# Optimization experiments

Hardware: AMD Instinct MI355X
Metric: run time of the kernel (lower is better)

Reference implementation:

```python
import jax, jax.numpy as jnp
import numpy as np

N_HEAD = 4

def setup_inputs() -> dict:
    key = jax.random.key(0)
    ks = jax.random.split(key, 10)
    B, N, C = 4, 16384, 256
    s = 1.0 / np.sqrt(C)
    inp = {
        'x': jax.random.normal(ks[0], (B, N, C), dtype=jnp.float32),
        'mask_x': jnp.ones((B, N), dtype=jnp.float32),
        'mask_y': jnp.ones((B, N), dtype=jnp.float32),
        'Wq': jax.random.normal(ks[1], (C, C), dtype=jnp.float32) * s,
        'bq': jnp.zeros((C,), dtype=jnp.float32),
        'Wk': jax.random.normal(ks[2], (C, C), dtype=jnp.float32) * s,
        'bk': jnp.zeros((C,), dtype=jnp.float32),
        'Wv': jax.random.normal(ks[3], (C, C), dtype=jnp.float32) * s,
        'bv': jnp.zeros((C,), dtype=jnp.float32),
        'Wp': jax.random.normal(ks[4], (C, C), dtype=jnp.float32) * s,
        'bp': jnp.zeros((C,), dtype=jnp.float32),
    }
    return inp

def reference(x, mask_x, mask_y, Wq, bq, Wk, bk, Wv, bv, Wp, bp):
    B, N, C = x.shape
    H = N_HEAD
    D = C // H
    # projections (y = x, self-attention path); weights stored [in, out]
    def split_heads(t):  # [B,N,C] -> [B,H,N,D]
        return t.reshape(B, N, H, D).transpose(0, 2, 1, 3)
    Q = split_heads(x @ Wq + bq)
    K = split_heads(x @ Wk + bk)
    V = split_heads(x @ Wv + bv)
    mx = mask_x[:, None, :, None]  # [B,1,N,1]
    my = mask_y[:, None, :, None]  # [B,1,M,1]
    K = K * my
    V = V * my
    # torch F.gelu default is exact (erf) gelu
    Q = jax.nn.gelu(Q, approximate=False) + 1.0
    K = jax.nn.gelu(K, approximate=False) + 1.0
    KV = jnp.einsum('bhmd,bhme->bhde', K, V)          # [B,H,D,D]
    K_sum = K.sum(axis=2, keepdims=True)               # [B,H,1,D]
    denom = jnp.sum(Q * K_sum, axis=-1, keepdims=True) # [B,H,N,1]
    attn_out = jnp.einsum('bhnd,bhde->bhne', Q, KV) / denom
    attn_out = attn_out * mx
    out = attn_out.transpose(0, 2, 1, 3).reshape(B, N, C)
    return out @ Wp + bp
```

## Files before the change

### kernel.cpp

```cpp
#include <hip/hip_runtime.h>
#include <hip/hip_bf16.h>
#include <cstdint>
#include <cstddef>

#define SEQ   16384
#define CHN   256

typedef __attribute__((ext_vector_type(8))) short  short8;
typedef __attribute__((ext_vector_type(4))) float  f32x4;

static __device__ __forceinline__ unsigned short f2bf(float f) {
    unsigned int u = __builtin_bit_cast(unsigned int, f);
    u += 0x7fffu + ((u >> 16) & 1u);
    return (unsigned short)(u >> 16);
}
static __device__ __forceinline__ float bf2f(unsigned short h) {
    unsigned int u = ((unsigned int)h) << 16;
    return __builtin_bit_cast(float, u);
}
static __device__ __forceinline__ float gelu_exact(float x) {
    return 0.5f * x * (1.0f + erff(x * 0.70710678118654752f));
}
static __device__ __forceinline__ int swz_us(int row, int kbyte) {
    return (row * 128 + (kbyte ^ ((row & 7) << 4))) >> 1;
}
static __device__ __forceinline__ int swzA(int row, int kbyte) {
    return (row * 512 + (kbyte ^ ((row & 7) << 4))) >> 1;
}

__global__ __launch_bounds__(256) void prep_kernel(
    const float* __restrict__ Wq, const float* __restrict__ Wk,
    const float* __restrict__ Wv, const float* __restrict__ Wp,
    unsigned short* __restrict__ Wqt, unsigned short* __restrict__ Wkt,
    unsigned short* __restrict__ Wvt, unsigned short* __restrict__ Wpt,
    float* __restrict__ KV, float* __restrict__ Ksum)
{
    const int idx = blockIdx.x * 256 + threadIdx.x;
    const int n = idx >> 8, k = idx & 255;
    const int src = k * 256 + n;
    Wqt[idx] = f2bf(Wq[src]);
    Wkt[idx] = f2bf(Wk[src]);
    Wvt[idx] = f2bf(Wv[src]);
    Wpt[idx] = f2bf(Wp[src]);
    KV[idx] = 0.0f;
    if (idx < 1024) Ksum[idx] = 0.0f;
}

__global__ __launch_bounds__(256) void qkv_gemm(
    const float* __restrict__ x, const float* __restrict__ my,
    const unsigned short* __restrict__ Wqt, const unsigned short* __restrict__ Wkt,
    const unsigned short* __restrict__ Wvt,
    const float* __restrict__ bq, const float* __restrict__ bk,
    const float* __restrict__ bv,
    unsigned short* __restrict__ Qb, unsigned short* __restrict__ Kb,
    unsigned short* __restrict__ Vb)
{
    __shared__ unsigned short As[128 * 256];
    __shared__ float mys[128];
    const int t = threadIdx.x;
    const long row0 = (long)blockIdx.x * 128;
    const int lane = t & 63, wave = t >> 6, wm = wave >> 1, wn = wave & 1;

    #pragma unroll
    for (int it = 0; it < 32; ++it) {
        const int idx = it * 256 + t;
        const int r = idx >> 6, c4 = (idx & 63) * 4;
        const float4 v = *(const float4*)(x + (row0 + r) * 256 + c4);
        uint2 pk;
        pk.x = (unsigned int)f2bf(v.x) | ((unsigned int)f2bf(v.y) << 16);
        pk.y = (unsigned int)f2bf(v.z) | ((unsigned int)f2bf(v.w) << 16);
        *(uint2*)&As[swzA(r, c4 * 2)] = pk;
    }
    if (t < 128) mys[t] = my[row0 + t];
    __syncthreads();

    #pragma unroll 1
    for (int ot = 0; ot < 6; ++ot) {
        const int mat  = ot >> 1;
        const int col0 = (ot & 1) * 128;
        const unsigned short* Wt = (mat == 0) ? Wqt : (mat == 1) ? Wkt : Wvt;
        const float* bias        = (mat == 0) ? bq  : (mat == 1) ? bk  : bv;
        unsigned short* Ob       = (mat == 0) ? Qb  : (mat == 1) ? Kb  : Vb;

        f32x4 acc[4][4];
        #pragma unroll
        for (int i = 0; i < 4; ++i)
            #pragma unroll
            for (int j = 0; j < 4; ++j) acc[i][j] = (f32x4)0.0f;

        #pragma unroll
        for (int kk = 0; kk < 8; ++kk) {
            const int ke = kk * 32 + (lane >> 4) * 8;
            short8 af[4], bfr[4];
            #pragma unroll
            for (int mi = 0; mi < 4; ++mi) {
                const int r = wm * 64 + mi * 16 + (lane & 15);
                af[mi] = *(const short8*)&As[swzA(r, ke * 2)];
            }
            #pragma unroll
            for (int ni = 0; ni < 4; ++ni) {
                const int n = col0 + wn * 64 + ni * 16 + (lane & 15);
                bfr[ni] = *(const short8*)(Wt + (size_t)n * 256 + ke);
            }
            #pragma unroll
            for (int mi = 0; mi < 4; ++mi)
                #pragma unroll
                for (int ni = 0; ni < 4; ++ni)
                    acc[mi][ni] = __builtin_amdgcn_mfma_f32_16x16x32_bf16(
                        af[mi], bfr[ni], acc[mi][ni], 0, 0, 0);
        }

        #pragma unroll
        for (int ni = 0; ni < 4; ++ni) {
            const int coll = col0 + wn * 64 + ni * 16 + (lane & 15);
            const float bc = bias[coll];
            #pragma unroll
            for (int mi = 0; mi < 4; ++mi) {
                const int lr0 = wm * 64 + mi * 16 + ((lane >> 4) << 2);
                #pragma unroll
                for (int r = 0; r < 4; ++r) {
                    const int lr = lr0 + r;
                    float val = acc[mi][ni][r] + bc;
                    if (mat == 0)      val = gelu_exact(val) + 1.0f;
                    else if (mat == 1) val = gelu_exact(val * mys[lr]) + 1.0f;
                    else               val = val * mys[lr];
                    Ob[(row0 + lr) * 256 + coll] = f2bf(val);
                }
            }
        }
    }
}

__global__ __launch_bounds__(256) void kv_reduce(
    const unsigned short* __restrict__ Kb, const unsigned short* __restrict__ Vb,
    float* __restrict__ KV, float* __restrict__ Ksum)
{
    __shared__ float kf[16][64];
    __shared__ float vf[16][64];
    const int t = threadIdx.x;
    const int bh = blockIdx.y;
    const long base = (long)(bh >> 2) * SEQ * 256 + (bh & 3) * 64;
    const long m0 = (long)blockIdx.x * 256;
    const int d0 = (t >> 4) * 4, e0 = (t & 15) * 4;
    const int sr = t >> 4, swhich = (t >> 3) & 1, sseg = t & 7;
    float acc[4][4] = {};
    float ks[4] = {};
    for (int it = 0; it < 16; ++it) {
        const long row = m0 + it * 16 + sr;
        const unsigned short* src = (swhich ? Vb : Kb) + base + row * 256 + sseg * 8;
        const uint4 raw = *(const uint4*)src;
        const unsigned short* rh = (const unsigned short*)&raw;
        float* dst = swhich ? &vf[sr][sseg * 8] : &kf[sr][sseg * 8];
        #pragma unroll
        for (int j = 0; j < 8; ++j) dst[j] = bf2f(rh[j]);
        __syncthreads();
        #pragma unroll
        for (int mm = 0; mm < 16; ++mm) {
            const float4 kd = *(const float4*)&kf[mm][d0];
            const float4 ve = *(const float4*)&vf[mm][e0];
            const float k4[4] = {kd.x, kd.y, kd.z, kd.w};
            const float v4[4] = {ve.x, ve.y, ve.z, ve.w};
            #pragma unroll
            for (int i = 0; i < 4; ++i)
                #pragma unroll
                for (int j = 0; j < 4; ++j) acc[i][j] += k4[i] * v4[j];
            if ((t & 15) == 0) {
                #pragma unroll
                for (int i = 0; i < 4; ++i) ks[i] += k4[i];
            }
        }
        __syncthreads();
    }
    #pragma unroll
    for (int i = 0; i < 4; ++i)
        #pragma unroll
        for (int j = 0; j < 4; ++j)
            atomicAdd(&KV[((size_t)bh * 64 + d0 + i) * 64 + e0 + j], acc[i][j]);
    if ((t & 15) == 0) {
        #pragma unroll
        for (int i = 0; i < 4; ++i) atomicAdd(&Ksum[bh * 64 + d0 + i], ks[i]);
    }
}

__global__ __launch_bounds__(256) void attn_kernel(
    const unsigned short* __restrict__ Qb, const float* __restrict__ KV,
    const float* __restrict__ Ksum, const float* __restrict__ mx,
    unsigned short* __restrict__ Ab)
{
    __shared__ unsigned short Qs[128 * 64];
    __shared__ unsigned short KVT[64 * 64];
    __shared__ float ksh[64];
    __shared__ float sden[128];
    const int t = threadIdx.x;
    const long row0 = (long)blockIdx.x * 128;
    const int b = (int)(row0 >> 14);
    const int lane = t & 63, wave = t >> 6, wm = wave >> 1, wn = wave & 1;

    for (int h = 0; h < 4; ++h) {
        const int bh = b * 4 + h;
        #pragma unroll
        for (int it = 0; it < 4; ++it) {
            const int idx = it * 256 + t;
            const int r = idx >> 3, c8 = (idx & 7) * 8;
            const uint4 v = *(const uint4*)(Qb + (row0 + r) * 256 + h * 64 + c8);
            *(uint4*)&Qs[swz_us(r, c8 * 2)] = v;
        }
        {
            const int e = t & 63, dg = t >> 6;
            #pragma unroll
            for (int i = 0; i < 16; ++i) {
                const int d = dg * 16 + i;
                const float v = KV[((size_t)bh * 64 + d) * 64 + e];
                KVT[(e * 128 + ((d * 2) ^ ((e & 7) << 4))) >> 1] = f2bf(v);
            }
        }
        if (t < 64) ksh[t] = Ksum[bh * 64 + t];
        __syncthreads();
        if (t < 128) {
            float s = 0.0f;
            for (int d = 0; d < 64; ++d)
                s += bf2f(Qs[swz_us(t, d * 2)]) * ksh[d];
            sden[t] = mx[row0 + t] / s;
        }
        __syncthreads();
        f32x4 acc[4][2];
        #pragma unroll
        for (int i = 0; i < 4; ++i) { acc[i][0] = (f32x4)0.0f; acc[i][1] = (f32x4)0.0f; }
        #pragma unroll
        for (int kk = 0; kk < 2; ++kk) {
            const int kbyte = kk * 64 + (lane >> 4) * 16;
            short8 af[4], bfr[2];
            #pragma unroll
            for (int mi = 0; mi < 4; ++mi) {
                const int r = wm * 64 + mi * 16 + (lane & 15);
                af[mi] = *(const short8*)&Qs[swz_us(r, kbyte)];
            }
            #pragma unroll
            for (int ni = 0; ni < 2; ++ni) {
                const int e = wn * 32 + ni * 16 + (lane & 15);
                bfr[ni] = *(const short8*)&KVT[swz_us(e, kbyte)];
            }
            #pragma unroll
            for (int mi = 0; mi < 4; ++mi)
                #pragma unroll
                for (int ni = 0; ni < 2; ++ni)
                    acc[mi][ni] = __builtin_amdgcn_mfma_f32_16x16x32_bf16(
                        af[mi], bfr[ni], acc[mi][ni], 0, 0, 0);
        }
        #pragma unroll
        for (int ni = 0; ni < 2; ++ni) {
            const int e = wn * 32 + ni * 16 + (lane & 15);
            #pragma unroll
            for (int mi = 0; mi < 4; ++mi) {
                const int lr0 = wm * 64 + mi * 16 + ((lane >> 4) << 2);
                #pragma unroll
                for (int r = 0; r < 4; ++r) {
                    const int lr = lr0 + r;
                    const float val = acc[mi][ni][r] * sden[lr];
                    Ab[(row0 + lr) * 256 + h * 64 + e] = f2bf(val);
                }
            }
        }
        __syncthreads();
    }
}

__global__ __launch_bounds__(256) void proj_gemm(
    const unsigned short* __restrict__ Ab, const unsigned short* __restrict__ Wpt,
    const float* __restrict__ bp, float* __restrict__ out)
{
    __shared__ unsigned short As[128 * 256];
    const int t = threadIdx.x;
    const long row0 = (long)blockIdx.x * 128;
    const int lane = t & 63, wave = t >> 6, wm = wave >> 1, wn = wave & 1;

    #pragma unroll
    for (int it = 0; it < 16; ++it) {
        const int idx = it * 256 + t;
        const int r = idx >> 5, c8 = (idx & 31) * 8;
        const uint4 v = *(const uint4*)(Ab + (row0 + r) * 256 + c8);
        *(uint4*)&As[swzA(r, c8 * 2)] = v;
    }
    __syncthreads();

    #pragma unroll 1
    for (int ct = 0; ct < 2; ++ct) {
        const int col0 = ct * 128;
        f32x4 acc[4][4];
        #pragma unroll
        for (int i = 0; i < 4; ++i)
            #pragma unroll
            for (int j = 0; j < 4; ++j) acc[i][j] = (f32x4)0.0f;

        #pragma unroll
        for (int kk = 0; kk < 8; ++kk) {
            const int ke = kk * 32 + (lane >> 4) * 8;
            short8 af[4], bfr[4];
            #pragma unroll
            for (int mi = 0; mi < 4; ++mi) {
                const int r = wm * 64 + mi * 16 + (lane & 15);
                af[mi] = *(const short8*)&As[swzA(r, ke * 2)];
            }
            #pragma unroll
            for (int ni = 0; ni < 4; ++ni) {
                const int n = col0 + wn * 64 + ni * 16 + (lane & 15);
                bfr[ni] = *(const short8*)(Wpt + (size_t)n * 256 + ke);
            }
            #pragma unroll
            for (int mi = 0; mi < 4; ++mi)
                #pragma unroll
                for (int ni = 0; ni < 4; ++ni)
                    acc[mi][ni] = __builtin_amdgcn_mfma_f32_16x16x32_bf16(
                        af[mi], bfr[ni], acc[mi][ni], 0, 0, 0);
        }

        #pragma unroll
        for (int ni = 0; ni < 4; ++ni) {
            const int coll = col0 + wn * 64 + ni * 16 + (lane & 15);
            const float bc = bp[coll];
            #pragma unroll
            for (int mi = 0; mi < 4; ++mi) {
                const int lr0 = wm * 64 + mi * 16 + ((lane >> 4) << 2);
                #pragma unroll
                for (int r = 0; r < 4; ++r) {
                    const long grow = row0 + lr0 + r;
                    out[grow * 256 + coll] = acc[mi][ni][r] + bc;
                }
            }
        }
    }
}

extern "C" void kernel_launch(void* const* d_in, const int* in_sizes, int n_in,
                              void* d_out, int out_size, void* d_ws, size_t ws_size,
                              hipStream_t stream)
{
    (void)in_sizes; (void)n_in; (void)out_size; (void)ws_size;
    const float* x  = (const float*)d_in[0];
    const float* mx = (const float*)d_in[1];
    const float* my = (const float*)d_in[2];
    const float* Wq = (const float*)d_in[3];
    const float* bq = (const float*)d_in[4];
    const float* Wk = (const float*)d_in[5];
    const float* bk = (const float*)d_in[6];
    const float* Wv = (const float*)d_in[7];
    const float* bv = (const float*)d_in[8];
    const float* Wp = (const float*)d_in[9];
    const float* bp = (const float*)d_in[10];
    float* out = (float*)d_out;

    const size_t nelem = (size_t)4 * SEQ * CHN;
    char* w = (char*)d_ws;
    unsigned short* Qb  = (unsigned short*)w; w += nelem * 2;
    unsigned short* Kb  = (unsigned short*)w; w += nelem * 2;
    unsigned short* Vb  = (unsigned short*)w; w += nelem * 2;
    unsigned short* Wqt = (unsigned short*)w; w += 131072;
    unsigned short* Wkt = (unsigned short*)w; w += 131072;
    unsigned short* Wvt = (unsigned short*)w; w += 131072;
    unsigned short* Wpt = (unsigned short*)w; w += 131072;
    float* KV   = (float*)w; w += 262144;
    float* Ksum = (float*)w; w += 4096;
    unsigned short* Ab = Kb;

    prep_kernel<<<256, 256, 0, stream>>>(Wq, Wk, Wv, Wp, Wqt, Wkt, Wvt, Wpt, KV, Ksum);
    qkv_gemm<<<512, 256, 0, stream>>>(x, my, Wqt, Wkt, Wvt, bq, bk, bv, Qb, Kb, Vb);
    kv_reduce<<<dim3(64, 16), 256, 0, stream>>>(Kb, Vb, KV, Ksum);
    attn_kernel<<<512, 256, 0, stream>>>(Qb, KV, Ksum, mx, Ab);
    proj_gemm<<<512, 256, 0, stream>>>(Ab, Wpt, bp, out);
}
```

Measured before the change: 416.4 us.

## Retile QKV and projection GEMMs with K-looped LDS tiles via global_load_lds

Adds a separate kernel that converts x to bf16 up front. The QKV and projection GEMMs are retiled so each workgroup computes one 128x128 output tile. Operand blocks of A and B (128x64 each) are staged into LDS per K step using global_load_lds, replacing the full-row A tile in LDS and direct global loads of the weights. Workgroups are interleaved across the 8 XCD slots and the grids grow to 3072 and 1024 blocks, to raise occupancy through smaller LDS use and to improve cache locality. The trade-offs are an extra write and read of x in bf16, repeated A-tile loads for each column tile, and LDS tiles with no swizzle that may cause bank conflicts.

After: 349.9 us. 1.19x faster.

```diff
diff --git a/kernel.cpp b/kernel.cpp
--- a/kernel.cpp
+++ b/kernel.cpp
@@ -9,6 +9,12 @@
 typedef __attribute__((ext_vector_type(8))) short  short8;
 typedef __attribute__((ext_vector_type(4))) float  f32x4;
 
+#define AS1 __attribute__((address_space(1)))
+#define AS3 __attribute__((address_space(3)))
+static __device__ __forceinline__ void gl_lds16(const void* g, void* l) {
+    __builtin_amdgcn_global_load_lds((const AS1 void*)g, (AS3 void*)l, 16, 0, 0);
+}
+
 static __device__ __forceinline__ unsigned short f2bf(float f) {
     unsigned int u = __builtin_bit_cast(unsigned int, f);
     u += 0x7fffu + ((u >> 16) & 1u);
@@ -24,83 +30,94 @@
 static __device__ __forceinline__ int swz_us(int row, int kbyte) {
     return (row * 128 + (kbyte ^ ((row & 7) << 4))) >> 1;
 }
-static __device__ __forceinline__ int swzA(int row, int kbyte) {
-    return (row * 512 + (kbyte ^ ((row & 7) << 4))) >> 1;
+
+__global__ __launch_bounds__(256) void cvt_kernel(
+    const float* __restrict__ x, unsigned short* __restrict__ xb)
+{
+    const int t0 = blockIdx.x * 256 + threadIdx.x;
+    #pragma unroll
+    for (int i = 0; i < 4; ++i) {
+        const long g = (long)t0 + (long)i * 524288;
+        const float4 a = *(const float4*)(x + g * 8);
+        const float4 b = *(const float4*)(x + g * 8 + 4);
+        uint4 pk;
+        pk.x = (unsigned int)f2bf(a.x) | ((unsigned int)f2bf(a.y) << 16);
+        pk.y = (unsigned int)f2bf(a.z) | ((unsigned int)f2bf(a.w) << 16);
+        pk.z = (unsigned int)f2bf(b.x) | ((unsigned int)f2bf(b.y) << 16);
+        pk.w = (unsigned int)f2bf(b.z) | ((unsigned int)f2bf(b.w) << 16);
+        *(uint4*)(xb + g * 8) = pk;
+    }
 }
 
 __global__ __launch_bounds__(256) void prep_kernel(
     const float* __restrict__ Wq, const float* __restrict__ Wk,
     const float* __restrict__ Wv, const float* __restrict__ Wp,
-    unsigned short* __restrict__ Wqt, unsigned short* __restrict__ Wkt,
-    unsigned short* __restrict__ Wvt, unsigned short* __restrict__ Wpt,
+    unsigned short* __restrict__ Wcat, unsigned short* __restrict__ Wpt,
     float* __restrict__ KV, float* __restrict__ Ksum)
 {
     const int idx = blockIdx.x * 256 + threadIdx.x;
     const int n = idx >> 8, k = idx & 255;
     const int src = k * 256 + n;
-    Wqt[idx] = f2bf(Wq[src]);
-    Wkt[idx] = f2bf(Wk[src]);
-    Wvt[idx] = f2bf(Wv[src]);
-    Wpt[idx] = f2bf(Wp[src]);
+    Wcat[idx]          = f2bf(Wq[src]);
+    Wcat[65536 + idx]  = f2bf(Wk[src]);
+    Wcat[131072 + idx] = f2bf(Wv[src]);
+    Wpt[idx]           = f2bf(Wp[src]);
     KV[idx] = 0.0f;
     if (idx < 1024) Ksum[idx] = 0.0f;
 }
 
 __global__ __launch_bounds__(256) void qkv_gemm(
-    const float* __restrict__ x, const float* __restrict__ my,
-    const unsigned short* __restrict__ Wqt, const unsigned short* __restrict__ Wkt,
-    const unsigned short* __restrict__ Wvt,
+    const unsigned short* __restrict__ xb, const float* __restrict__ my,
+    const unsigned short* __restrict__ Wcat,
     const float* __restrict__ bq, const float* __restrict__ bk,
     const float* __restrict__ bv,
     unsigned short* __restrict__ Qb, unsigned short* __restrict__ Kb,
     unsigned short* __restrict__ Vb)
 {
-    __shared__ unsigned short As[128 * 256];
+    __shared__ unsigned short As[128 * 64];
+    __shared__ unsigned short Bs[128 * 64];
     __shared__ float mys[128];
     const int t = threadIdx.x;
-    const long row0 = (long)blockIdx.x * 128;
+    const int nwg = 3072, phys = blockIdx.x;
+    const int l = (phys & 7) * (nwg >> 3) + (phys >> 3);
+    const int rt = l / 6, ct = l % 6;
+    const long row0 = (long)rt * 128;
+    const int  ncol0 = ct * 128;
+    const int  mat = ct >> 1;
     const int lane = t & 63, wave = t >> 6, wm = wave >> 1, wn = wave & 1;
 
-    #pragma unroll
-    for (int it = 0; it < 32; ++it) {
-        const int idx = it * 256 + t;
-        const int r = idx >> 6, c4 = (idx & 63) * 4;
-        const float4 v = *(const float4*)(x + (row0 + r) * 256 + c4);
-        uint2 pk;
-        pk.x = (unsigned int)f2bf(v.x) | ((unsigned int)f2bf(v.y) << 16);
-        pk.y = (unsigned int)f2bf(v.z) | ((unsigned int)f2bf(v.w) << 16);
-        *(uint2*)&As[swzA(r, c4 * 2)] = pk;
-    }
     if (t < 128) mys[t] = my[row0 + t];
-    __syncthreads();
-
-    #pragma unroll 1
-    for (int ot = 0; ot < 6; ++ot) {
-        const int mat  = ot >> 1;
-        const int col0 = (ot & 1) * 128;
-        const unsigned short* Wt = (mat == 0) ? Wqt : (mat == 1) ? Wkt : Wvt;
-        const float* bias        = (mat == 0) ? bq  : (mat == 1) ? bk  : bv;
-        unsigned short* Ob       = (mat == 0) ? Qb  : (mat == 1) ? Kb  : Vb;
-
-        f32x4 acc[4][4];
-        #pragma unroll
-        for (int i = 0; i < 4; ++i)
-            #pragma unroll
-            for (int j = 0; j < 4; ++j) acc[i][j] = (f32x4)0.0f;
-
-        #pragma unroll
-        for (int kk = 0; kk < 8; ++kk) {
-            const int ke = kk * 32 + (lane >> 4) * 8;
+
+    f32x4 acc[4][4];
+    #pragma unroll
+    for (int i = 0; i < 4; ++i)
+        #pragma unroll
+        for (int j = 0; j < 4; ++j) acc[i][j] = (f32x4)0.0f;
+
+    for (int k0 = 0; k0 < 256; k0 += 64) {
+        #pragma unroll
+        for (int i = 0; i < 4; ++i) {
+            const int c = i * 256 + t;
+            gl_lds16(xb + (row0 + (c >> 3)) * 256 + k0 + (c & 7) * 8, &As[c * 8]);
+        }
+        #pragma unroll
+        for (int i = 0; i < 4; ++i) {
+            const int c = i * 256 + t;
+            gl_lds16(Wcat + (size_t)(ncol0 + (c >> 3)) * 256 + k0 + (c & 7) * 8, &Bs[c * 8]);
+        }
+        __syncthreads();
+        #pragma unroll
+        for (int kk = 0; kk < 2; ++kk) {
             short8 af[4], bfr[4];
             #pragma unroll
             for (int mi = 0; mi < 4; ++mi) {
                 const int r = wm * 64 + mi * 16 + (lane & 15);
-                af[mi] = *(const short8*)&As[swzA(r, ke * 2)];
+                af[mi] = *(const short8*)&As[r * 64 + kk * 32 + (lane >> 4) * 8];
             }
             #pragma unroll
             for (int ni = 0; ni < 4; ++ni) {
-                const int n = col0 + wn * 64 + ni * 16 + (lane & 15);
-                bfr[ni] = *(const short8*)(Wt + (size_t)n * 256 + ke);
+                const int n = wn * 64 + ni * 16 + (lane & 15);
+                bfr[ni] = *(const short8*)&Bs[n * 64 + kk * 32 + (lane >> 4) * 8];
             }
             #pragma unroll
             for (int mi = 0; mi < 4; ++mi)
@@ -109,23 +126,27 @@
                     acc[mi][ni] = __builtin_amdgcn_mfma_f32_16x16x32_bf16(
                         af[mi], bfr[ni], acc[mi][ni], 0, 0, 0);
         }
-
-        #pragma unroll
-        for (int ni = 0; ni < 4; ++ni) {
-            const int coll = col0 + wn * 64 + ni * 16 + (lane & 15);
-            const float bc = bias[coll];
-            #pragma unroll
-            for (int mi = 0; mi < 4; ++mi) {
-                const int lr0 = wm * 64 + mi * 16 + ((lane >> 4) << 2);
-                #pragma unroll
-                for (int r = 0; r < 4; ++r) {
-                    const int lr = lr0 + r;
-                    float val = acc[mi][ni][r] + bc;
-                    if (mat == 0)      val = gelu_exact(val) + 1.0f;
-                    else if (mat == 1) val = gelu_exact(val * mys[lr]) + 1.0f;
-                    else               val = val * mys[lr];
-                    Ob[(row0 + lr) * 256 + coll] = f2bf(val);
-                }
+        __syncthreads();
+    }
+
+    const float* bias  = (mat == 0) ? bq : (mat == 1) ? bk : bv;
+    unsigned short* Ob = (mat == 0) ? Qb : (mat == 1) ? Kb : Vb;
+    const int col0 = (ct & 1) * 128;
+    #pragma unroll
+    for (int ni = 0; ni < 4; ++ni) {
+        const int coll = col0 + wn * 64 + ni * 16 + (lane & 15);
+        const float bc = bias[coll];
+        #pragma unroll
+        for (int mi = 0; mi < 4; ++mi) {
+            const int lr0 = wm * 64 + mi * 16 + ((lane >> 4) << 2);
+            #pragma unroll
+            for (int r = 0; r < 4; ++r) {
+                const int lr = lr0 + r;
+                float val = acc[mi][ni][r] + bc;
+                if (mat == 0)      val = gelu_exact(val) + 1.0f;
+                else if (mat == 1) val = gelu_exact(val * mys[lr]) + 1.0f;
+                else               val = val * mys[lr];
+                Ob[(row0 + lr) * 256 + coll] = f2bf(val);
             }
         }
     }
@@ -269,42 +290,46 @@
     const unsigned short* __restrict__ Ab, const unsigned short* __restrict__ Wpt,
     const float* __restrict__ bp, float* __restrict__ out)
 {
-    __shared__ unsigned short As[128 * 256];
+    __shared__ unsigned short As[128 * 64];
+    __shared__ unsigned short Bs[128 * 64];
     const int t = threadIdx.x;
-    const long row0 = (long)blockIdx.x * 128;
+    const int nwg = 1024, phys = blockIdx.x;
+    const int l = (phys & 7) * (nwg >> 3) + (phys >> 3);
+    const int rt = l >> 1, ct = l & 1;
+    const long row0 = (long)rt * 128;
+    const int col0 = ct * 128;
     const int lane = t & 63, wave = t >> 6, wm = wave >> 1, wn = wave & 1;
 
-    #pragma unroll
-    for (int it = 0; it < 16; ++it) {
-        const int idx = it * 256 + t;
-        const int r = idx >> 5, c8 = (idx & 31) * 8;
-        const uint4 v = *(const uint4*)(Ab + (row0 + r) * 256 + c8);
-        *(uint4*)&As[swzA(r, c8 * 2)] = v;
-    }
-    __syncthreads();
-
-    #pragma unroll 1
-    for (int ct = 0; ct < 2; ++ct) {
-        const int col0 = ct * 128;
-        f32x4 acc[4][4];
-        #pragma unroll
-        for (int i = 0; i < 4; ++i)
-            #pragma unroll
-            for (int j = 0; j < 4; ++j) acc[i][j] = (f32x4)0.0f;
-
-        #pragma unroll
-        for (int kk = 0; kk < 8; ++kk) {
-            const int ke = kk * 32 + (lane >> 4) * 8;
+    f32x4 acc[4][4];
+    #pragma unroll
+    for (int i = 0; i < 4; ++i)
+        #pragma unroll
+        for (int j = 0; j < 4; ++j) acc[i][j] = (f32x4)0.0f;
+
+    for (int k0 = 0; k0 < 256; k0 += 64) {
+        #pragma unroll
+        for (int i = 0; i < 4; ++i) {
+            const int c = i * 256 + t;
+            gl_lds16(Ab + (row0 + (c >> 3)) * 256 + k0 + (c & 7) * 8, &As[c * 8]);
+        }
+        #pragma unroll
+        for (int i = 0; i < 4; ++i) {
+            const int c = i * 256 + t;
+            gl_lds16(Wpt + (size_t)(col0 + (c >> 3)) * 256 + k0 + (c & 7) * 8, &Bs[c * 8]);
+        }
+        __syncthreads();
+        #pragma unroll
+        for (int kk = 0; kk < 2; ++kk) {
             short8 af[4], bfr[4];
             #pragma unroll
             for (int mi = 0; mi < 4; ++mi) {
                 const int r = wm * 64 + mi * 16 + (lane & 15);
-                af[mi] = *(const short8*)&As[swzA(r, ke * 2)];
+                af[mi] = *(const short8*)&As[r * 64 + kk * 32 + (lane >> 4) * 8];
             }
             #pragma unroll
             for (int ni = 0; ni < 4; ++ni) {
-                const int n = col0 + wn * 64 + ni * 16 + (lane & 15);
-                bfr[ni] = *(const short8*)(Wpt + (size_t)n * 256 + ke);
+                const int n = wn * 64 + ni * 16 + (lane & 15);
+                bfr[ni] = *(const short8*)&Bs[n * 64 + kk * 32 + (lane >> 4) * 8];
             }
             #pragma unroll
             for (int mi = 0; mi < 4; ++mi)
@@ -313,19 +338,19 @@
                     acc[mi][ni] = __builtin_amdgcn_mfma_f32_16x16x32_bf16(
                         af[mi], bfr[ni], acc[mi][ni], 0, 0, 0);
         }
-
-        #pragma unroll
-        for (int ni = 0; ni < 4; ++ni) {
-            const int coll = col0 + wn * 64 + ni * 16 + (lane & 15);
-            const float bc = bp[coll];
-            #pragma unroll
-            for (int mi = 0; mi < 4; ++mi) {
-                const int lr0 = wm * 64 + mi * 16 + ((lane >> 4) << 2);
-                #pragma unroll
-                for (int r = 0; r < 4; ++r) {
-                    const long grow = row0 + lr0 + r;
-                    out[grow * 256 + coll] = acc[mi][ni][r] + bc;
-                }
+        __syncthreads();
+    }
+    #pragma unroll
+    for (int ni = 0; ni < 4; ++ni) {
+        const int coll = col0 + wn * 64 + ni * 16 + (lane & 15);
+        const float bc = bp[coll];
+        #pragma unroll
+        for (int mi = 0; mi < 4; ++mi) {
+            const int lr0 = wm * 64 + mi * 16 + ((lane >> 4) << 2);
+            #pragma unroll
+            for (int r = 0; r < 4; ++r) {
+                const long grow = row0 + lr0 + r;
+                out[grow * 256 + coll] = acc[mi][ni][r] + bc;
             }
         }
     }
@@ -351,20 +376,20 @@
 
     const size_t nelem = (size_t)4 * SEQ * CHN;
     char* w = (char*)d_ws;
-    unsigned short* Qb  = (unsigned short*)w; w += nelem * 2;
-    unsigned short* Kb  = (unsigned short*)w; w += nelem * 2;
-    unsigned short* Vb  = (unsigned short*)w; w += nelem * 2;
-    unsigned short* Wqt = (unsigned short*)w; w += 131072;
-    unsigned short* Wkt = (unsigned short*)w; w += 131072;
-    unsigned short* Wvt = (unsigned short*)w; w += 131072;
-    unsigned short* Wpt = (unsigned short*)w; w += 131072;
+    unsigned short* xb   = (unsigned short*)w; w += nelem * 2;
+    unsigned short* Qb   = (unsigned short*)w; w += nelem * 2;
+    unsigned short* Kb   = (unsigned short*)w; w += nelem * 2;
+    unsigned short* Vb   = (unsigned short*)w; w += nelem * 2;
+    unsigned short* Wcat = (unsigned short*)w; w += 768 * 256 * 2;
+    unsigned short* Wpt  = (unsigned short*)w; w += 131072;
     float* KV   = (float*)w; w += 262144;
     float* Ksum = (float*)w; w += 4096;
     unsigned short* Ab = Kb;
 
-    prep_kernel<<<256, 256, 0, stream>>>(Wq, Wk, Wv, Wp, Wqt, Wkt, Wvt, Wpt, KV, Ksum);
-    qkv_gemm<<<512, 256, 0, stream>>>(x, my, Wqt, Wkt, Wvt, bq, bk, bv, Qb, Kb, Vb);
+    cvt_kernel<<<2048, 256, 0, stream>>>(x, xb);
+    prep_kernel<<<256, 256, 0, stream>>>(Wq, Wk, Wv, Wp, Wcat, Wpt, KV, Ksum);
+    qkv_gemm<<<3072, 256, 0, stream>>>(xb, my, Wcat, bq, bk, bv, Qb, Kb, Vb);
     kv_reduce<<<dim3(64, 16), 256, 0, stream>>>(Kb, Vb, KV, Ksum);
     attn_kernel<<<512, 256, 0, stream>>>(Qb, KV, Ksum, mx, Ab);
-    proj_gemm<<<512, 256, 0, stream>>>(Ab, Wpt, bp, out);
-}
+    proj_gemm<<<1024, 256, 0, stream>>>(Ab, Wpt, bp, out);
+}
```
